# Kernel tuning notes

Hardware: AMD Instinct MI355X
Metric: run time of the kernel (lower is better)

The kernel has to match this reference:

```python
import jax, jax.numpy as jnp
import numpy as np

B, S, E, H = 4, 1024, 1024, 16
HD = E // H


def setup_inputs() -> dict:
    key = jax.random.key(0)
    ks = jax.random.split(key, 5)
    x = jax.random.normal(ks[0], (B, S, E), dtype=jnp.float32)
    # causal mask: True = masked (filled with -inf), as in masked_fill_
    mask = jnp.triu(jnp.ones((S, S), dtype=bool), k=1)
    in_proj_weight = jax.random.normal(ks[1], (3 * E, E), dtype=jnp.float32) * (E ** -0.5)
    in_proj_bias = jax.random.normal(ks[2], (3 * E,), dtype=jnp.float32) * 0.02
    out_w = jax.random.normal(ks[3], (E, E), dtype=jnp.float32) * (E ** -0.5)
    out_b = jax.random.normal(ks[4], (E,), dtype=jnp.float32) * 0.02
    return {"x": x, "mask": mask, "in_proj_weight": in_proj_weight,
            "in_proj_bias": in_proj_bias, "out_w": out_w, "out_b": out_b}


def reference(x, mask, in_proj_weight, in_proj_bias, out_w, out_b):
    scaling = HD ** -0.5
    # fused QKV projection (self-attention path: qkv_same)
    qkv = jnp.einsum('bse,fe->bsf', x, in_proj_weight) + in_proj_bias  # [B,S,3E]
    q, k, v = jnp.split(qkv, 3, axis=-1)
    # split heads -> [B,H,S,HD]
    def heads(t):
        return t.reshape(B, S, H, HD).transpose(0, 2, 1, 3)
    q, k, v = heads(q), heads(k), heads(v)
    scores = jnp.einsum('bhsd,bhtd->bhst', q, k) * scaling  # [B,H,S,S]
    scores = jnp.where(mask[None, None, :, :], -jnp.inf, scores)
    att = jax.nn.softmax(scores, axis=-1)  # dropout p=0.0 (eval)
    out = jnp.einsum('bhst,bhtd->bhsd', att, v)  # [B,H,S,HD]
    out = out.transpose(0, 2, 1, 3).reshape(B, S, E)  # concat heads
    out = jnp.einsum('bse,fe->bsf', out, out_w) + out_b
    att_weights = att.reshape(B * H, S, S)
    return out, att_weights
```

## Files before the change

kernel.cpp:

```cpp
#include <hip/hip_runtime.h>
#include <hip/hip_bf16.h>
#include <stdint.h>

#define NH 16
#define SEQ 1024
#define EMB 1024
#define HDIM 64
#define BATCH 4
#define SPAD 1032

typedef float f32x4 __attribute__((ext_vector_type(4)));
typedef short bf16x8 __attribute__((ext_vector_type(8)));

static __device__ __forceinline__ short f2bf(float f) {
  union { float f; uint32_t u; } v; v.f = f;
  uint32_t r = (v.u + 0x7FFF + ((v.u >> 16) & 1)) >> 16;
  return (short)(uint16_t)r;
}
static __device__ __forceinline__ float bf2f(short h) {
  union { uint32_t u; float f; } v; v.u = ((uint32_t)(uint16_t)h) << 16;
  return v.f;
}

static __device__ __forceinline__ void gload_lds16(const void* g, void* l) {
  __builtin_amdgcn_global_load_lds(
      (const __attribute__((address_space(1))) void*)g,
      (__attribute__((address_space(3))) void*)l, 16, 0, 0);
}

static __device__ __forceinline__ void cvt8(const float* s, short* d) {
  const float4* sv = (const float4*)s;
  float4 a = sv[0], b = sv[1];
  bf16x8 o;
  o[0] = f2bf(a.x); o[1] = f2bf(a.y); o[2] = f2bf(a.z); o[3] = f2bf(a.w);
  o[4] = f2bf(b.x); o[5] = f2bf(b.y); o[6] = f2bf(b.z); o[7] = f2bf(b.w);
  *(bf16x8*)d = o;
}

__global__ void cvt3_kernel(const float* __restrict__ x, const float* __restrict__ w,
                            const float* __restrict__ o, short* __restrict__ xb,
                            short* __restrict__ wb, short* __restrict__ ob) {
  int i = (blockIdx.x * blockDim.x + threadIdx.x) * 8;
  if (i < 4194304) {
    cvt8(x + i, xb + i);
  } else if (i < 7340032) {
    cvt8(w + (i - 4194304), wb + (i - 4194304));
  } else {
    cvt8(o + (i - 7340032), ob + (i - 7340032));
  }
}

__global__ __launch_bounds__(256) void transpose_v(const short* __restrict__ v,
                                                   short* __restrict__ vt) {
  __shared__ short t[64][72];
  const int tid = threadIdx.x;
  const int bh = blockIdx.y;
  const int sb = blockIdx.x * 64;
  const int row = tid >> 2;
  const int c0 = (tid & 3) * 16;
  const short* src = v + ((size_t)(bh * SEQ + sb + row)) * HDIM + c0;
  *(bf16x8*)&t[row][c0] = *(const bf16x8*)src;
  *(bf16x8*)&t[row][c0 + 8] = *(const bf16x8*)(src + 8);
  __syncthreads();
  bf16x8 o0, o1;
#pragma unroll
  for (int i = 0; i < 8; ++i) o0[i] = t[c0 + i][row];
#pragma unroll
  for (int i = 0; i < 8; ++i) o1[i] = t[c0 + 8 + i][row];
  short* dst = vt + ((size_t)(bh * HDIM + row)) * SEQ + sb + c0;
  *(bf16x8*)dst = o0;
  *(bf16x8*)(dst + 8) = o1;
}

__global__ __launch_bounds__(256) void gemm_qkv(
    const short* __restrict__ A, const short* __restrict__ Bm,
    const float* __restrict__ bias, short* __restrict__ qkvws) {
  __shared__ short As[128 * 64];
  __shared__ short Bs[128 * 64];
  const int tid = threadIdx.x;
  const int w = tid >> 6, l = tid & 63;
  const int l15 = l & 15, l4 = l >> 4;
  const int wr = w >> 1, wc = w & 1;
  const int row0 = blockIdx.x * 128;
  const int col0 = blockIdx.y * 128;
  const int K = EMB;

  f32x4 acc[4][4] = {};

  const int o = (w * 4) * 1024 + l * 16;
  for (int k0 = 0; k0 < K; k0 += 64) {
#pragma unroll
    for (int c = 0; c < 4; ++c) {
      int oo = o + c * 1024;
      int row = oo >> 7;
      int colb = oo & 127;
      int scol = colb ^ ((row & 7) << 4);
      gload_lds16((const char*)A + ((size_t)(row0 + row) * K + k0) * 2 + scol,
                  (char*)As + (w * 4 + c) * 1024);
      gload_lds16((const char*)Bm + ((size_t)(col0 + row) * K + k0) * 2 + scol,
                  (char*)Bs + (w * 4 + c) * 1024);
    }
    __syncthreads();
#pragma unroll
    for (int kk = 0; kk < 2; ++kk) {
      bf16x8 af[4], bfr[4];
      const int kb = (kk * 64 + l4 * 16) ^ ((l15 & 7) << 4);
#pragma unroll
      for (int i = 0; i < 4; ++i) {
        af[i] = *(const bf16x8*)((const char*)As + (wr * 64 + i * 16 + l15) * 128 + kb);
        bfr[i] = *(const bf16x8*)((const char*)Bs + (wc * 64 + i * 16 + l15) * 128 + kb);
      }
#pragma unroll
      for (int i = 0; i < 4; ++i)
#pragma unroll
        for (int j = 0; j < 4; ++j)
          acc[i][j] = __builtin_amdgcn_mfma_f32_16x16x32_bf16(af[i], bfr[j], acc[i][j], 0, 0, 0);
    }
    __syncthreads();
  }

#pragma unroll
  for (int j = 0; j < 4; ++j) {
    int f = col0 + wc * 64 + j * 16 + l15;
    float bv = bias[f];
    int part = f >> 10;
    int e = f & 1023;
    int hh = e >> 6, d = e & 63;
#pragma unroll
    for (int i = 0; i < 4; ++i) {
#pragma unroll
      for (int rr = 0; rr < 4; ++rr) {
        int m = row0 + wr * 64 + i * 16 + l4 * 4 + rr;
        int bb = m >> 10, ss = m & 1023;
        qkvws[(size_t)part * 4194304 +
              ((size_t)(bb * NH + hh) * SEQ + ss) * HDIM + d] =
            f2bf(acc[i][j][rr] + bv);
      }
    }
  }
}

__global__ __launch_bounds__(256) void gemm_out64(
    const short* __restrict__ A, const short* __restrict__ Bm,
    const float* __restrict__ bias, float* __restrict__ outp) {
  __shared__ short As[128 * 64];
  __shared__ short Bs[64 * 64];
  const int tid = threadIdx.x;
  const int w = tid >> 6, l = tid & 63;
  const int l15 = l & 15, l4 = l >> 4;
  const int row0 = blockIdx.x * 128;
  const int col0 = blockIdx.y * 64;
  const int K = EMB;

  f32x4 acc[2][4] = {};

  const int oA = (w * 4) * 1024 + l * 16;
  const int oB = (w * 2) * 1024 + l * 16;
  for (int k0 = 0; k0 < K; k0 += 64) {
#pragma unroll
    for (int c = 0; c < 4; ++c) {
      int oo = oA + c * 1024;
      int row = oo >> 7;
      int colb = oo & 127;
      int scol = colb ^ ((row & 7) << 4);
      gload_lds16((const char*)A + ((size_t)(row0 + row) * K + k0) * 2 + scol,
                  (char*)As + (w * 4 + c) * 1024);
    }
#pragma unroll
    for (int c = 0; c < 2; ++c) {
      int oo = oB + c * 1024;
      int row = oo >> 7;
      int colb = oo & 127;
      int scol = colb ^ ((row & 7) << 4);
      gload_lds16((const char*)Bm + ((size_t)(col0 + row) * K + k0) * 2 + scol,
                  (char*)Bs + (w * 2 + c) * 1024);
    }
    __syncthreads();
#pragma unroll
    for (int kk = 0; kk < 2; ++kk) {
      bf16x8 af[2], bfr[4];
      const int kb = (kk * 64 + l4 * 16) ^ ((l15 & 7) << 4);
#pragma unroll
      for (int i = 0; i < 2; ++i)
        af[i] = *(const bf16x8*)((const char*)As + (w * 32 + i * 16 + l15) * 128 + kb);
#pragma unroll
      for (int j = 0; j < 4; ++j)
        bfr[j] = *(const bf16x8*)((const char*)Bs + (j * 16 + l15) * 128 + kb);
#pragma unroll
      for (int i = 0; i < 2; ++i)
#pragma unroll
        for (int j = 0; j < 4; ++j)
          acc[i][j] = __builtin_amdgcn_mfma_f32_16x16x32_bf16(af[i], bfr[j], acc[i][j], 0, 0, 0);
    }
    __syncthreads();
  }

#pragma unroll
  for (int j = 0; j < 4; ++j) {
    int f = col0 + j * 16 + l15;
    float bv = bias[f];
#pragma unroll
    for (int i = 0; i < 2; ++i)
#pragma unroll
      for (int rr = 0; rr < 4; ++rr) {
        int m = row0 + w * 32 + i * 16 + l4 * 4 + rr;
        __builtin_nontemporal_store(acc[i][j][rr] + bv, &outp[(size_t)m * EMB + f]);
      }
  }
}

__global__ __launch_bounds__(256) void attn_kernel(
    const short* __restrict__ qws, const short* __restrict__ kws,
    const short* __restrict__ vtws, float* __restrict__ attg,
    short* __restrict__ aow) {
  __shared__ short strip[32 * SPAD];
  __shared__ float wsum[4][32];
  __shared__ float inv_sum[32];

  const int tid = threadIdx.x;
  const int w = tid >> 6, l = tid & 63;
  const int l15 = l & 15, l4 = l >> 4;
  const int blk = blockIdx.x;
  const int bh = blk >> 5;
  const int r = blk & 31;
  const int rowbase = r * 32;

  const short* qb = qws + ((size_t)bh * SEQ + rowbase) * HDIM;
  const short* kb = kws + (size_t)bh * SEQ * HDIM;
  const short* vb = vtws + (size_t)bh * HDIM * SEQ;

  bf16x8 qf[2][2];
#pragma unroll
  for (int rg = 0; rg < 2; ++rg)
#pragma unroll
    for (int ks = 0; ks < 2; ++ks)
      qf[rg][ks] = *(const bf16x8*)(qb + (rg * 16 + l15) * HDIM + ks * 32 + l4 * 8);

  const int ngroups = (rowbase + 32) >> 4;
  float psum[2][4] = {};

  for (int g = w; g < ngroups; g += 4) {
    const short* kg = kb + (g * 16 + l15) * HDIM + l4 * 8;
    bf16x8 kf0 = *(const bf16x8*)(kg);
    bf16x8 kf1 = *(const bf16x8*)(kg + 32);
    f32x4 a0 = {}, a1 = {};
    a0 = __builtin_amdgcn_mfma_f32_16x16x32_bf16(qf[0][0], kf0, a0, 0, 0, 0);
    a0 = __builtin_amdgcn_mfma_f32_16x16x32_bf16(qf[0][1], kf1, a0, 0, 0, 0);
    a1 = __builtin_amdgcn_mfma_f32_16x16x32_bf16(qf[1][0], kf0, a1, 0, 0, 0);
    a1 = __builtin_amdgcn_mfma_f32_16x16x32_bf16(qf[1][1], kf1, a1, 0, 0, 0);
    int col = g * 16 + l15;
#pragma unroll
    for (int rg = 0; rg < 2; ++rg) {
#pragma unroll
      for (int rr = 0; rr < 4; ++rr) {
        int rloc = rg * 16 + l4 * 4 + rr;
        int row = rowbase + rloc;
        float sv = (rg ? a1[rr] : a0[rr]) * 0.125f;
        float ev = (col <= row) ? __expf(sv) : 0.0f;
        psum[rg][rr] += ev;
        strip[rloc * SPAD + col] = f2bf(ev);
      }
    }
  }

#pragma unroll
  for (int rg = 0; rg < 2; ++rg)
#pragma unroll
    for (int rr = 0; rr < 4; ++rr) {
      float v = psum[rg][rr];
      v += __shfl_xor(v, 1);
      v += __shfl_xor(v, 2);
      v += __shfl_xor(v, 4);
      v += __shfl_xor(v, 8);
      psum[rg][rr] = v;
    }
  if (l15 == 0) {
#pragma unroll
    for (int rg = 0; rg < 2; ++rg)
#pragma unroll
      for (int rr = 0; rr < 4; ++rr)
        wsum[w][rg * 16 + l4 * 4 + rr] = psum[rg][rr];
  }
  __syncthreads();
  if (tid < 32) {
    float s = wsum[0][tid] + wsum[1][tid] + wsum[2][tid] + wsum[3][tid];
    inv_sum[tid] = 1.0f / s;
  }
  __syncthreads();

  {
    const int limit = ngroups * 16;
    const int rloc = tid >> 3;
    const int cb = tid & 7;
    float* arow = attg + (size_t)bh * SEQ * SEQ + (size_t)(rowbase + rloc) * SEQ;
    float isr = inv_sum[rloc];
#pragma unroll
    for (int i = 0; i < 16; ++i) {
      int c = (cb + i * 8) * 8;
      f32x4 o0, o1;
      if (c < limit) {
        bf16x8 p = *(const bf16x8*)&strip[rloc * SPAD + c];
        o0[0] = bf2f(p[0]) * isr; o0[1] = bf2f(p[1]) * isr;
        o0[2] = bf2f(p[2]) * isr; o0[3] = bf2f(p[3]) * isr;
        o1[0] = bf2f(p[4]) * isr; o1[1] = bf2f(p[5]) * isr;
        o1[2] = bf2f(p[6]) * isr; o1[3] = bf2f(p[7]) * isr;
      } else {
        o0 = (f32x4)0.0f;
        o1 = (f32x4)0.0f;
      }
      __builtin_nontemporal_store(o0, (f32x4*)(arow + c));
      __builtin_nontemporal_store(o1, (f32x4*)(arow + c + 4));
    }
  }

  {
    const int nch = ngroups >> 1;
    const int d0 = w * 16;
    f32x4 oacc[2] = {};
    const short* vrow = vb + (d0 + l15) * SEQ + l4 * 8;
    for (int c = 0; c < nch; ++c) {
      bf16x8 vf = *(const bf16x8*)(vrow + c * 32);
      bf16x8 p0 = *(const bf16x8*)&strip[(0 + l15) * SPAD + c * 32 + l4 * 8];
      bf16x8 p1 = *(const bf16x8*)&strip[(16 + l15) * SPAD + c * 32 + l4 * 8];
      oacc[0] = __builtin_amdgcn_mfma_f32_16x16x32_bf16(p0, vf, oacc[0], 0, 0, 0);
      oacc[1] = __builtin_amdgcn_mfma_f32_16x16x32_bf16(p1, vf, oacc[1], 0, 0, 0);
    }
    const int b = bh >> 4, h = bh & 15;
#pragma unroll
    for (int rg = 0; rg < 2; ++rg) {
#pragma unroll
      for (int rr = 0; rr < 4; ++rr) {
        int rloc = rg * 16 + l4 * 4 + rr;
        int s = rowbase + rloc;
        float v = oacc[rg][rr] * inv_sum[rloc];
        aow[((size_t)(b * SEQ + s)) * EMB + h * HDIM + d0 + l15] = f2bf(v);
      }
    }
  }
}

extern "C" void kernel_launch(void* const* d_in, const int* in_sizes, int n_in,
                              void* d_out, int out_size, void* d_ws, size_t ws_size,
                              hipStream_t stream) {
  (void)in_sizes; (void)n_in; (void)out_size; (void)ws_size;
  const float* x = (const float*)d_in[0];
  const float* ipw = (const float*)d_in[2];
  const float* ipb = (const float*)d_in[3];
  const float* ow = (const float*)d_in[4];
  const float* ob = (const float*)d_in[5];
  float* outp = (float*)d_out;
  float* attg = (float*)d_out + (size_t)BATCH * SEQ * EMB;

  char* ws = (char*)d_ws;
  short* xbf = (short*)(ws);
  short* wbf = (short*)(ws + 8388608);
  short* owbf = (short*)(ws + 14680064);
  short* qkvws = (short*)(ws + 16777216);
  short* aow = (short*)(ws + 41943040);
  short* vtws = (short*)(ws);

  short* qws = qkvws;
  short* kws = qkvws + 4194304;
  short* vws = qkvws + 8388608;

  cvt3_kernel<<<4096, 256, 0, stream>>>(x, ipw, ow, xbf, wbf, owbf);

  dim3 g1(32, 24);
  gemm_qkv<<<g1, 256, 0, stream>>>(xbf, wbf, ipb, qkvws);

  transpose_v<<<dim3(16, 64), 256, 0, stream>>>(vws, vtws);

  attn_kernel<<<2048, 256, 0, stream>>>(qws, kws, vtws, attg, aow);

  gemm_out64<<<dim3(32, 16), 256, 0, stream>>>(aow, owbf, ob, outp);
}
```

Measured before the change: 184.6 us.

## Double-buffer LDS in both GEMMs and halve attention row tile to 16

Both GEMM kernels now keep two LDS buffers and issue the next K-tile's global-to-LDS loads before computing on the current one, so memory latency can overlap with MFMA work. The attention kernel handles 16 query rows per block instead of 32 and launches twice as many blocks. That gives finer causal-work granularity, better load balance and a smaller LDS strip, which should raise occupancy. The cost is doubled GEMM LDS use, which may lower GEMM occupancy, and attention blocks that reuse each K/V load for fewer rows.

```diff
diff --git a/kernel.cpp b/kernel.cpp
--- a/kernel.cpp
+++ b/kernel.cpp
@@ -72,11 +72,24 @@
   *(bf16x8*)(dst + 8) = o1;
 }
 
+#define STAGE_QKV(bb, kk0)                                                     \
+  {                                                                            \
+    _Pragma("unroll") for (int c = 0; c < 4; ++c) {                            \
+      int oo = o + c * 1024;                                                   \
+      int row = oo >> 7;                                                       \
+      int scol = (oo & 127) ^ ((row & 7) << 4);                                \
+      gload_lds16((const char*)A + ((size_t)(row0 + row) * K + (kk0)) * 2 + scol, \
+                  (char*)As[bb] + (w * 4 + c) * 1024);                         \
+      gload_lds16((const char*)Bm + ((size_t)(col0 + row) * K + (kk0)) * 2 + scol,\
+                  (char*)Bs[bb] + (w * 4 + c) * 1024);                         \
+    }                                                                          \
+  }
+
 __global__ __launch_bounds__(256) void gemm_qkv(
     const short* __restrict__ A, const short* __restrict__ Bm,
     const float* __restrict__ bias, short* __restrict__ qkvws) {
-  __shared__ short As[128 * 64];
-  __shared__ short Bs[128 * 64];
+  __shared__ short As[2][128 * 64];
+  __shared__ short Bs[2][128 * 64];
   const int tid = threadIdx.x;
   const int w = tid >> 6, l = tid & 63;
   const int l15 = l & 15, l4 = l >> 4;
@@ -88,27 +101,20 @@
   f32x4 acc[4][4] = {};
 
   const int o = (w * 4) * 1024 + l * 16;
+  STAGE_QKV(0, 0);
+  __syncthreads();
+
+  int cur = 0;
   for (int k0 = 0; k0 < K; k0 += 64) {
-#pragma unroll
-    for (int c = 0; c < 4; ++c) {
-      int oo = o + c * 1024;
-      int row = oo >> 7;
-      int colb = oo & 127;
-      int scol = colb ^ ((row & 7) << 4);
-      gload_lds16((const char*)A + ((size_t)(row0 + row) * K + k0) * 2 + scol,
-                  (char*)As + (w * 4 + c) * 1024);
-      gload_lds16((const char*)Bm + ((size_t)(col0 + row) * K + k0) * 2 + scol,
-                  (char*)Bs + (w * 4 + c) * 1024);
-    }
-    __syncthreads();
+    if (k0 + 64 < K) STAGE_QKV(cur ^ 1, k0 + 64);
 #pragma unroll
     for (int kk = 0; kk < 2; ++kk) {
       bf16x8 af[4], bfr[4];
       const int kb = (kk * 64 + l4 * 16) ^ ((l15 & 7) << 4);
 #pragma unroll
       for (int i = 0; i < 4; ++i) {
-        af[i] = *(const bf16x8*)((const char*)As + (wr * 64 + i * 16 + l15) * 128 + kb);
-        bfr[i] = *(const bf16x8*)((const char*)Bs + (wc * 64 + i * 16 + l15) * 128 + kb);
+        af[i] = *(const bf16x8*)((const char*)As[cur] + (wr * 64 + i * 16 + l15) * 128 + kb);
+        bfr[i] = *(const bf16x8*)((const char*)Bs[cur] + (wc * 64 + i * 16 + l15) * 128 + kb);
       }
 #pragma unroll
       for (int i = 0; i < 4; ++i)
@@ -117,6 +123,7 @@
           acc[i][j] = __builtin_amdgcn_mfma_f32_16x16x32_bf16(af[i], bfr[j], acc[i][j], 0, 0, 0);
     }
     __syncthreads();
+    cur ^= 1;
   }
 
 #pragma unroll
@@ -140,11 +147,29 @@
   }
 }
 
+#define STAGE_OUT(bb, kk0)                                                     \
+  {                                                                            \
+    _Pragma("unroll") for (int c = 0; c < 4; ++c) {                            \
+      int oo = oA + c * 1024;                                                  \
+      int row = oo >> 7;                                                       \
+      int scol = (oo & 127) ^ ((row & 7) << 4);                                \
+      gload_lds16((const char*)A + ((size_t)(row0 + row) * K + (kk0)) * 2 + scol, \
+                  (char*)As[bb] + (w * 4 + c) * 1024);                         \
+    }                                                                          \
+    _Pragma("unroll") for (int c = 0; c < 2; ++c) {                            \
+      int oo = oB + c * 1024;                                                  \
+      int row = oo >> 7;                                                       \
+      int scol = (oo & 127) ^ ((row & 7) << 4);                                \
+      gload_lds16((const char*)Bm + ((size_t)(col0 + row) * K + (kk0)) * 2 + scol,\
+                  (char*)Bs[bb] + (w * 2 + c) * 1024);                         \
+    }                                                                          \
+  }
+
 __global__ __launch_bounds__(256) void gemm_out64(
     const short* __restrict__ A, const short* __restrict__ Bm,
     const float* __restrict__ bias, float* __restrict__ outp) {
-  __shared__ short As[128 * 64];
-  __shared__ short Bs[64 * 64];
+  __shared__ short As[2][128 * 64];
+  __shared__ short Bs[2][64 * 64];
   const int tid = threadIdx.x;
   const int w = tid >> 6, l = tid & 63;
   const int l15 = l & 15, l4 = l >> 4;
@@ -156,36 +181,22 @@
 
   const int oA = (w * 4) * 1024 + l * 16;
   const int oB = (w * 2) * 1024 + l * 16;
+  STAGE_OUT(0, 0);
+  __syncthreads();
+
+  int cur = 0;
   for (int k0 = 0; k0 < K; k0 += 64) {
-#pragma unroll
-    for (int c = 0; c < 4; ++c) {
-      int oo = oA + c * 1024;
-      int row = oo >> 7;
-      int colb = oo & 127;
-      int scol = colb ^ ((row & 7) << 4);
-      gload_lds16((const char*)A + ((size_t)(row0 + row) * K + k0) * 2 + scol,
-                  (char*)As + (w * 4 + c) * 1024);
-    }
-#pragma unroll
-    for (int c = 0; c < 2; ++c) {
-      int oo = oB + c * 1024;
-      int row = oo >> 7;
-      int colb = oo & 127;
-      int scol = colb ^ ((row & 7) << 4);
-      gload_lds16((const char*)Bm + ((size_t)(col0 + row) * K + k0) * 2 + scol,
-                  (char*)Bs + (w * 2 + c) * 1024);
-    }
-    __syncthreads();
+    if (k0 + 64 < K) STAGE_OUT(cur ^ 1, k0 + 64);
 #pragma unroll
     for (int kk = 0; kk < 2; ++kk) {
       bf16x8 af[2], bfr[4];
       const int kb = (kk * 64 + l4 * 16) ^ ((l15 & 7) << 4);
 #pragma unroll
       for (int i = 0; i < 2; ++i)
-        af[i] = *(const bf16x8*)((const char*)As + (w * 32 + i * 16 + l15) * 128 + kb);
+        af[i] = *(const bf16x8*)((const char*)As[cur] + (w * 32 + i * 16 + l15) * 128 + kb);
 #pragma unroll
       for (int j = 0; j < 4; ++j)
-        bfr[j] = *(const bf16x8*)((const char*)Bs + (j * 16 + l15) * 128 + kb);
+        bfr[j] = *(const bf16x8*)((const char*)Bs[cur] + (j * 16 + l15) * 128 + kb);
 #pragma unroll
       for (int i = 0; i < 2; ++i)
 #pragma unroll
@@ -193,6 +204,7 @@
           acc[i][j] = __builtin_amdgcn_mfma_f32_16x16x32_bf16(af[i], bfr[j], acc[i][j], 0, 0, 0);
     }
     __syncthreads();
+    cur ^= 1;
   }
 
 #pragma unroll
@@ -213,90 +225,79 @@
     const short* __restrict__ qws, const short* __restrict__ kws,
     const short* __restrict__ vtws, float* __restrict__ attg,
     short* __restrict__ aow) {
-  __shared__ short strip[32 * SPAD];
-  __shared__ float wsum[4][32];
-  __shared__ float inv_sum[32];
+  __shared__ short strip[16 * SPAD];
+  __shared__ float wsum[4][16];
+  __shared__ float inv_sum[16];
 
   const int tid = threadIdx.x;
   const int w = tid >> 6, l = tid & 63;
   const int l15 = l & 15, l4 = l >> 4;
   const int blk = blockIdx.x;
-  const int bh = blk >> 5;
-  const int r = blk & 31;
-  const int rowbase = r * 32;
+  const int bh = blk >> 6;
+  const int r = blk & 63;
+  const int rowbase = r * 16;
 
   const short* qb = qws + ((size_t)bh * SEQ + rowbase) * HDIM;
   const short* kb = kws + (size_t)bh * SEQ * HDIM;
   const short* vb = vtws + (size_t)bh * HDIM * SEQ;
 
-  bf16x8 qf[2][2];
-#pragma unroll
-  for (int rg = 0; rg < 2; ++rg)
-#pragma unroll
-    for (int ks = 0; ks < 2; ++ks)
-      qf[rg][ks] = *(const bf16x8*)(qb + (rg * 16 + l15) * HDIM + ks * 32 + l4 * 8);
-
-  const int ngroups = (rowbase + 32) >> 4;
-  float psum[2][4] = {};
-
-  for (int g = w; g < ngroups; g += 4) {
+  bf16x8 qf[2];
+#pragma unroll
+  for (int ks = 0; ks < 2; ++ks)
+    qf[ks] = *(const bf16x8*)(qb + l15 * HDIM + ks * 32 + l4 * 8);
+
+  const int ng2 = (r + 2) & ~1;
+  float psum[4] = {};
+
+  for (int g = w; g < ng2; g += 4) {
     const short* kg = kb + (g * 16 + l15) * HDIM + l4 * 8;
     bf16x8 kf0 = *(const bf16x8*)(kg);
     bf16x8 kf1 = *(const bf16x8*)(kg + 32);
-    f32x4 a0 = {}, a1 = {};
-    a0 = __builtin_amdgcn_mfma_f32_16x16x32_bf16(qf[0][0], kf0, a0, 0, 0, 0);
-    a0 = __builtin_amdgcn_mfma_f32_16x16x32_bf16(qf[0][1], kf1, a0, 0, 0, 0);
-    a1 = __builtin_amdgcn_mfma_f32_16x16x32_bf16(qf[1][0], kf0, a1, 0, 0, 0);
-    a1 = __builtin_amdgcn_mfma_f32_16x16x32_bf16(qf[1][1], kf1, a1, 0, 0, 0);
+    f32x4 a0 = {};
+    a0 = __builtin_amdgcn_mfma_f32_16x16x32_bf16(qf[0], kf0, a0, 0, 0, 0);
+    a0 = __builtin_amdgcn_mfma_f32_16x16x32_bf16(qf[1], kf1, a0, 0, 0, 0);
     int col = g * 16 + l15;
 #pragma unroll
-    for (int rg = 0; rg < 2; ++rg) {
-#pragma unroll
-      for (int rr = 0; rr < 4; ++rr) {
-        int rloc = rg * 16 + l4 * 4 + rr;
-        int row = rowbase + rloc;
-        float sv = (rg ? a1[rr] : a0[rr]) * 0.125f;
-        float ev = (col <= row) ? __expf(sv) : 0.0f;
-        psum[rg][rr] += ev;
-        strip[rloc * SPAD + col] = f2bf(ev);
-      }
-    }
-  }
-
-#pragma unroll
-  for (int rg = 0; rg < 2; ++rg)
-#pragma unroll
     for (int rr = 0; rr < 4; ++rr) {
-      float v = psum[rg][rr];
-      v += __shfl_xor(v, 1);
-      v += __shfl_xor(v, 2);
-      v += __shfl_xor(v, 4);
-      v += __shfl_xor(v, 8);
-      psum[rg][rr] = v;
-    }
+      int rloc = l4 * 4 + rr;
+      int row = rowbase + rloc;
+      float sv = a0[rr] * 0.125f;
+      float ev = (col <= row) ? __expf(sv) : 0.0f;
+      psum[rr] += ev;
+      strip[rloc * SPAD + col] = f2bf(ev);
+    }
+  }
+
+#pragma unroll
+  for (int rr = 0; rr < 4; ++rr) {
+    float v = psum[rr];
+    v += __shfl_xor(v, 1);
+    v += __shfl_xor(v, 2);
+    v += __shfl_xor(v, 4);
+    v += __shfl_xor(v, 8);
+    psum[rr] = v;
+  }
   if (l15 == 0) {
 #pragma unroll
-    for (int rg = 0; rg < 2; ++rg)
-#pragma unroll
-      for (int rr = 0; rr < 4; ++rr)
-        wsum[w][rg * 16 + l4 * 4 + rr] = psum[rg][rr];
-  }
-  __syncthreads();
-  if (tid < 32) {
+    for (int rr = 0; rr < 4; ++rr)
+      wsum[w][l4 * 4 + rr] = psum[rr];
+  }
+  __syncthreads();
+  if (tid < 16) {
     float s = wsum[0][tid] + wsum[1][tid] + wsum[2][tid] + wsum[3][tid];
     inv_sum[tid] = 1.0f / s;
   }
   __syncthreads();
 
   {
-    const int limit = ngroups * 16;
-    const int rloc = tid >> 3;
-    const int cb = tid & 7;
+    const int limit = ng2 * 16;
+    const int rloc = tid >> 4;
+    const int cb = tid & 15;
     float* arow = attg + (size_t)bh * SEQ * SEQ + (size_t)(rowbase + rloc) * SEQ;
     float isr = inv_sum[rloc];
 #pragma unroll
-    for (int i = 0; i < 16; ++i) {
-      int c = (cb + i * 8) * 8;
+    for (int i = 0; i < 8; ++i) {
+      int c = (cb + i * 16) * 8;
       f32x4 o0, o1;
       if (c < limit) {
         bf16x8 p = *(const bf16x8*)&strip[rloc * SPAD + c];
@@ -314,27 +315,22 @@
   }
 
   {
-    const int nch = ngroups >> 1;
+    const int nch = ng2 >> 1;
     const int d0 = w * 16;
-    f32x4 oacc[2] = {};
+    f32x4 oacc = {};
     const short* vrow = vb + (d0 + l15) * SEQ + l4 * 8;
     for (int c = 0; c < nch; ++c) {
       bf16x8 vf = *(const bf16x8*)(vrow + c * 32);
-      bf16x8 p0 = *(const bf16x8*)&strip[(0 + l15) * SPAD + c * 32 + l4 * 8];
-      bf16x8 p1 = *(const bf16x8*)&strip[(16 + l15) * SPAD + c * 32 + l4 * 8];
-      oacc[0] = __builtin_amdgcn_mfma_f32_16x16x32_bf16(p0, vf, oacc[0], 0, 0, 0);
-      oacc[1] = __builtin_amdgcn_mfma_f32_16x16x32_bf16(p1, vf, oacc[1], 0, 0, 0);
+      bf16x8 p0 = *(const bf16x8*)&strip[l15 * SPAD + c * 32 + l4 * 8];
+      oacc = __builtin_amdgcn_mfma_f32_16x16x32_bf16(p0, vf, oacc, 0, 0, 0);
     }
     const int b = bh >> 4, h = bh & 15;
 #pragma unroll
-    for (int rg = 0; rg < 2; ++rg) {
-#pragma unroll
-      for (int rr = 0; rr < 4; ++rr) {
-        int rloc = rg * 16 + l4 * 4 + rr;
-        int s = rowbase + rloc;
-        float v = oacc[rg][rr] * inv_sum[rloc];
-        aow[((size_t)(b * SEQ + s)) * EMB + h * HDIM + d0 + l15] = f2bf(v);
-      }
+    for (int rr = 0; rr < 4; ++rr) {
+      int rloc = l4 * 4 + rr;
+      int s = rowbase + rloc;
+      float v = oacc[rr] * inv_sum[rloc];
+      aow[((size_t)(b * SEQ + s)) * EMB + h * HDIM + d0 + l15] = f2bf(v);
     }
   }
 }
@@ -370,7 +366,7 @@
 
   transpose_v<<<dim3(16, 64), 256, 0, stream>>>(vws, vtws);
 
-  attn_kernel<<<2048, 256, 0, stream>>>(qws, kws, vtws, attg, aow);
+  attn_kernel<<<4096, 256, 0, stream>>>(qws, kws, vtws, attg, aow);
 
   gemm_out64<<<dim3(32, 16), 256, 0, stream>>>(aow, owbf, ob, outp);
 }
```

Measured after the change: 183.0 us. About the same (-0.9%).
